# Kernel optimization log

Hardware: AMD Instinct MI355X
Metric: run time of the kernel (lower is better)

Reference implementation:

```python
import jax, jax.numpy as jnp
import numpy as np

# Dims mirror cfg: hidden_dim=128, n_cluster=512; margin from cfg['memory_bank']
B, D, H, W = 64, 128, 64, 64
K = 512
MARGIN = 0.005
EPS = 1e-12  # F.normalize eps


def setup_inputs() -> dict:
    key = jax.random.key(0)
    k1, k2 = jax.random.split(key)
    x = jax.random.normal(k1, (B, D, H, W), dtype=jnp.float32)
    centroid = jax.random.normal(k2, (K, D), dtype=jnp.float32)
    return {"x": x, "centroid": centroid}


def _l2_normalize(v, axis=-1):
    n = jnp.sqrt(jnp.sum(v * v, axis=axis, keepdims=True))
    return v / jnp.maximum(n, EPS)


def reference(x, centroid):
    b, d, h, w = x.shape
    # _flatten: (b,d,h,w) -> (bhw, d)
    flat_raw = jnp.transpose(x, (0, 2, 3, 1)).reshape(-1, d)  # (N, d)
    norm_x = _l2_normalize(flat_raw)                          # (N, d), F.normalize(dim=-1)
    c_norm = _l2_normalize(centroid)                          # (K, d)

    dist = (jnp.sum(norm_x * norm_x, axis=1, keepdims=True)
            + jnp.sum(c_norm * c_norm, axis=1)
            - 2.0 * jnp.matmul(norm_x, c_norm.T))

    idx = jnp.argmin(dist, axis=-1)                           # (N,) hard assignment
    neg_top2, _ = jax.lax.top_k(-dist, 2)                     # torch.topk(-distance, k=2)
    gap = neg_top2[:, 0] - neg_top2[:, 1]                     # values[:,0]-values[:,1]
    above = gap > MARGIN                                      # margin mask

    # masked per-cluster scatter of the RAW features (the enqueue step),
    # expressed as a fixed-shape segment reduction instead of ragged queues.
    sel = jnp.where(above[:, None], flat_raw, 0.0)            # (N, d)
    cluster_sums = jax.ops.segment_sum(sel, idx, num_segments=K)            # (K, d)
    counts = jax.ops.segment_sum(above.astype(jnp.float32), idx, num_segments=K)  # (K,)

    # _reshape(norm_z1_1): (bhw, d) -> (b, d, h, w)
    out = jnp.transpose(norm_x.reshape(b, h, w, d), (0, 3, 1, 2))
    return out, cluster_sums, counts, idx
```

## Files before the change

### kernel.cpp

```cpp
#include <hip/hip_runtime.h>
#include <stdint.h>

#define D 128
#define K 512
#define HW 4096
#define NPIX 262144
#define OUT_NORM_ELEMS 33554432
#define MARGIN 0.005f
#define EPS 1e-12f
#define LOSCALE 2048.0f
#define RSCALE (1.0f / 2048.0f)

typedef _Float16 f16x8 __attribute__((ext_vector_type(8)));
typedef float f32x4 __attribute__((ext_vector_type(4)));
typedef float f32x2 __attribute__((ext_vector_type(2)));

#define FENCE() asm volatile("" ::: "memory")

__device__ __forceinline__ short f2h(float f) {
    _Float16 h = (_Float16)f; return *reinterpret_cast<short*>(&h);
}
__device__ __forceinline__ float h2f(short s) {
    _Float16 h = *reinterpret_cast<_Float16*>(&s); return (float)h;
}

__global__ void zero_kernel(float* __restrict__ p, int n) {
    int i = blockIdx.x * blockDim.x + threadIdx.x;
    if (i < n) p[i] = 0.0f;
}

__global__ void normalize_centroids(const float* __restrict__ c,
                                    short* __restrict__ csp,
                                    float* __restrict__ nc) {
    int k = blockIdx.x * 4 + (threadIdx.x >> 6);
    int lane = threadIdx.x & 63;
    float2 v = *(const float2*)(c + (size_t)k * D + lane * 2);
    float ss = v.x * v.x + v.y * v.y;
    #pragma unroll
    for (int off = 32; off; off >>= 1) ss += __shfl_xor(ss, off);
    float rinv = 1.0f / fmaxf(sqrtf(ss), EPS);
    float ox = v.x * rinv, oy = v.y * rinv;
    short hx = f2h(ox), hy = f2h(oy);
    short lx = f2h((ox - h2f(hx)) * LOSCALE);
    short ly = f2h((oy - h2f(hy)) * LOSCALE);
    *(short2*)&csp[(size_t)k * 256 + 2 * lane]       = make_short2(hx, hy);
    *(short2*)&csp[(size_t)k * 256 + 128 + 2 * lane] = make_short2(lx, ly);
    float ss2 = ox * ox + oy * oy;
    #pragma unroll
    for (int off = 32; off; off >>= 1) ss2 += __shfl_xor(ss2, off);
    if (lane == 0) nc[k] = ss2;
}

#define K1S 66
__global__ __launch_bounds__(256) void normalize_x(
    const float* __restrict__ x, float* __restrict__ out_norm,
    float* __restrict__ rows, int prim)
{
    __shared__ float xt[256 * K1S];
    const int t = threadIdx.x;
    const int pix0 = blockIdx.x * 256;
    const int b = pix0 >> 12;
    const int p0 = pix0 & (HW - 1);
    const float* xg = x + (size_t)b * (D * HW) + p0 + t;
    float* og = out_norm + (size_t)b * (D * HW) + p0 + t;

    float ss = 0.f;
    #pragma unroll 16
    for (int d = 0; d < D; ++d) { float v = xg[(size_t)d * HW]; ss += v * v; }
    float rinv = 1.f / fmaxf(sqrtf(ss), EPS);

    if (prim) {
        #pragma unroll
        for (int half = 0; half < 2; ++half) {
            const int d0 = half * 64;
            #pragma unroll 8
            for (int d = 0; d < 64; ++d) {
                float v = xg[(size_t)(d0 + d) * HW];
                og[(size_t)(d0 + d) * HW] = v * rinv;
                xt[t * K1S + d] = v;
            }
            __syncthreads();
            #pragma unroll
            for (int s = 0; s < 32; ++s) {
                int idx = s * 256 + t;
                int p = idx >> 5;
                int i = idx & 31;
                f32x2 v = *(f32x2*)&xt[p * K1S + 2 * i];
                *(f32x2*)&rows[(size_t)(pix0 + p) * 128 + d0 + 2 * i] = v;
            }
            __syncthreads();
        }
    } else {
        #pragma unroll 16
        for (int d = 0; d < D; ++d) {
            float v = xg[(size_t)d * HW];
            og[(size_t)d * HW] = v * rinv;
        }
    }
}

#define UPD(dd, cc, ri) do {                                      \
    bool lt1 = (dd) < d1[ri];                                     \
    float nd2 = lt1 ? d1[ri] : (((dd) < d2[ri]) ? (dd) : d2[ri]); \
    i1[ri] = lt1 ? (cc) : i1[ri];                                 \
    d1[ri] = lt1 ? (dd) : d1[ri];                                 \
    d2[ri] = nd2;                                                 \
} while (0)

#define SMBUF 8192
#define SMNC  32768
#define SM2_BYTES 34816
__global__ __launch_bounds__(512, 4) void gemm_top2(
    const float* __restrict__ xn, const float* __restrict__ rows,
    const short* __restrict__ csp, const float* __restrict__ nc,
    float* __restrict__ oidx, int* __restrict__ pixinfo, int prim)
{
    __shared__ char smem[SM2_BYTES] __attribute__((aligned(16)));
    float* nc_s = (float*)(smem + SMNC);

    const int t = threadIdx.x;
    const int lane = t & 63;
    const int wid = t >> 6;
    const int lb15 = lane & 15;
    const int kl4 = lane >> 4;
    const int kl = kl4 * 16;
    const int lswzB = lb15 << 4;
    const int pix0 = blockIdx.x * 256;

    nc_s[t] = nc[t];

    auto stageB = [&](int bufoff, int cb) {
        const char* src = (const char*)csp + (size_t)cb * 512;
        int Pl = wid * 1024 + lane * 16;
        int row = Pl >> 9;
        int goff = Pl ^ ((row & 15) << 4);
        __builtin_amdgcn_global_load_lds(
            (const __attribute__((address_space(1))) uint32_t*)(src + goff),
            (__attribute__((address_space(3))) uint32_t*)(smem + bufoff + Pl),
            16, 0, 0);
    };

    f16x8 ahi[2][4], alo[2][4];
    if (prim) {
        #pragma unroll
        for (int mf = 0; mf < 2; ++mf) {
            const float* rp = rows + (size_t)(pix0 + wid * 32 + mf * 16 + lb15) * 128;
            f32x4 v0[4], v1[4];
            float ss = 0.f;
            #pragma unroll
            for (int kq = 0; kq < 4; ++kq) {
                v0[kq] = *(const f32x4*)(rp + kq * 32 + kl4 * 8);
                v1[kq] = *(const f32x4*)(rp + kq * 32 + kl4 * 8 + 4);
                #pragma unroll
                for (int e = 0; e < 4; ++e)
                    ss += v0[kq][e] * v0[kq][e] + v1[kq][e] * v1[kq][e];
            }
            ss += __shfl_xor(ss, 16);
            ss += __shfl_xor(ss, 32);
            float rinv = 1.f / fmaxf(sqrtf(ss), EPS);
            #pragma unroll
            for (int kq = 0; kq < 4; ++kq) {
                f16x8 h, l;
                #pragma unroll
                for (int e = 0; e < 4; ++e) {
                    float a = v0[kq][e] * rinv;
                    _Float16 hv = (_Float16)a;
                    h[e] = hv; l[e] = (_Float16)((a - (float)hv) * LOSCALE);
                    float c = v1[kq][e] * rinv;
                    _Float16 hw = (_Float16)c;
                    h[4 + e] = hw; l[4 + e] = (_Float16)((c - (float)hw) * LOSCALE);
                }
                ahi[mf][kq] = h; alo[mf][kq] = l;
            }
        }
    } else {
        #pragma unroll
        for (int mf = 0; mf < 2; ++mf) {
            int px = pix0 + wid * 32 + mf * 16 + lb15;
            const float* xp = xn + (size_t)(px >> 12) * (D * HW) + (px & (HW - 1));
            #pragma unroll
            for (int kq = 0; kq < 4; ++kq) {
                f16x8 h, l;
                #pragma unroll
                for (int e = 0; e < 8; ++e) {
                    float v = xp[(size_t)(kq * 32 + kl4 * 8 + e) * HW];
                    _Float16 hv = (_Float16)v;
                    h[e] = hv;
                    l[e] = (_Float16)((v - (float)hv) * LOSCALE);
                }
                ahi[mf][kq] = h; alo[mf][kq] = l;
            }
        }
    }
    __syncthreads();

    stageB(0 * SMBUF, 0);
    stageB(1 * SMBUF, 16);

    float d1[8], d2[8]; int i1[8];
    #pragma unroll
    for (int r = 0; r < 8; ++r) { d1[r] = 3.4e38f; d2[r] = 3.4e38f; i1[r] = 0; }

    for (int c = 0; c < 32; ++c) {
        const int cb = c * 16;
        if (c + 2 < 32) stageB(((c + 2) & 3) * SMBUF, cb + 32);
        if (c < 30)      { asm volatile("s_waitcnt vmcnt(2)" ::: "memory"); }
        else if (c == 30){ asm volatile("s_waitcnt vmcnt(1)" ::: "memory"); }
        else             { asm volatile("s_waitcnt vmcnt(0)" ::: "memory"); }
        __builtin_amdgcn_s_barrier();
        FENCE();
        const int bufoff = (c & 3) * SMBUF;

        f32x4 am[2], ac[2];
        #pragma unroll
        for (int mf = 0; mf < 2; ++mf) {
            am[mf] = (f32x4){0.f, 0.f, 0.f, 0.f};
            ac[mf] = (f32x4){0.f, 0.f, 0.f, 0.f};
        }

        #pragma unroll
        for (int kq = 0; kq < 4; ++kq) {
            const int rowb = lb15 * 512;
            f16x8 bh = *(const f16x8*)(smem + bufoff + rowb + ((kq * 64 + kl) ^ lswzB));
            f16x8 bl = *(const f16x8*)(smem + bufoff + rowb + ((256 + kq * 64 + kl) ^ lswzB));
            #pragma unroll
            for (int mf = 0; mf < 2; ++mf) {
                am[mf] = __builtin_amdgcn_mfma_f32_16x16x32_f16(ahi[mf][kq], bh, am[mf], 0, 0, 0);
                ac[mf] = __builtin_amdgcn_mfma_f32_16x16x32_f16(ahi[mf][kq], bl, ac[mf], 0, 0, 0);
                ac[mf] = __builtin_amdgcn_mfma_f32_16x16x32_f16(alo[mf][kq], bh, ac[mf], 0, 0, 0);
            }
        }

        {
            int cid = cb + lb15;
            float ncv = nc_s[cid];
            #pragma unroll
            for (int mf = 0; mf < 2; ++mf)
                #pragma unroll
                for (int j = 0; j < 4; ++j) {
                    int ri = mf * 4 + j;
                    float dd = ncv - 2.f * am[mf][j] - (2.f * RSCALE) * ac[mf][j];
                    UPD(dd, cid, ri);
                }
        }
        FENCE();
    }

    #pragma unroll
    for (int r = 0; r < 8; ++r) {
        #pragma unroll
        for (int m = 1; m < 16; m <<= 1) {
            float o1 = __shfl_xor(d1[r], m);
            float o2 = __shfl_xor(d2[r], m);
            int   oi = __shfl_xor(i1[r], m);
            bool take = (o1 < d1[r]) || (o1 == d1[r] && oi < i1[r]);
            float loser = take ? d1[r] : o1;
            d2[r] = fminf(loser, fminf(d2[r], o2));
            if (take) { d1[r] = o1; i1[r] = oi; }
        }
    }
    if (lb15 == 0) {
        #pragma unroll
        for (int mf = 0; mf < 2; ++mf)
            #pragma unroll
            for (int j = 0; j < 4; ++j) {
                int r = mf * 4 + j;
                int px = pix0 + wid * 32 + mf * 16 + kl4 * 4 + j;
                oidx[px] = (float)i1[r];
                pixinfo[px] = (d2[r] - d1[r] > MARGIN) ? i1[r] : -1;
            }
    }
}

__global__ __launch_bounds__(256) void segsum_kernel(
    const float* __restrict__ x, const float* __restrict__ rows,
    const int* __restrict__ pixinfo, float* __restrict__ csum,
    float* __restrict__ ccnt, int prim)
{
    __shared__ float psum[4 * 128];
    __shared__ int pcnt[4];
    const int kc   = blockIdx.x >> 3;
    const int oct  = blockIdx.x & 7;
    const int lane = threadIdx.x & 63;
    const int w    = threadIdx.x >> 6;
    const int base = oct * 32768 + w * 8192;

    float a0 = 0.f, a1 = 0.f;
    int cnt = 0;
    for (int it = 0; it < 128; ++it) {
        int ibase = base + it * 64;
        int v = pixinfo[ibase + lane];
        unsigned long long m = __ballot(v == kc);
        cnt += (int)__popcll(m);
        while (m) {
            int bpos = __builtin_ctzll(m);
            m &= m - 1;
            int pid = ibase + bpos;
            if (prim) {
                f32x2 r = *(const f32x2*)(rows + (size_t)pid * 128 + 2 * lane);
                a0 += r.x;
                a1 += r.y;
            } else {
                const float* xp = x + ((size_t)(pid >> 12)) * (D * HW) + (pid & (HW - 1));
                a0 += xp[(size_t)(2 * lane) * HW];
                a1 += xp[(size_t)(2 * lane + 1) * HW];
            }
        }
    }
    psum[w * 128 + 2 * lane]     = a0;
    psum[w * 128 + 2 * lane + 1] = a1;
    if (lane == 0) pcnt[w] = cnt;
    __syncthreads();
    if (threadIdx.x < 128) {
        float s = psum[threadIdx.x] + psum[128 + threadIdx.x] +
                  psum[256 + threadIdx.x] + psum[384 + threadIdx.x];
        atomicAdd(&csum[(size_t)kc * D + threadIdx.x], s);
    }
    if (threadIdx.x == 0) {
        float c = (float)(pcnt[0] + pcnt[1] + pcnt[2] + pcnt[3]);
        atomicAdd(&ccnt[kc], c);
    }
}

extern "C" void kernel_launch(void* const* d_in, const int* in_sizes, int n_in,
                              void* d_out, int out_size, void* d_ws, size_t ws_size,
                              hipStream_t stream) {
    const float* x   = (const float*)d_in[0];
    const float* cen = (const float*)d_in[1];

    float* out      = (float*)d_out;
    float* out_norm = out;
    float* csum     = out + OUT_NORM_ELEMS;
    float* ccnt     = csum + (size_t)K * D;
    float* oidx     = ccnt + K;

    char* ws = (char*)d_ws;
    short* csp     = (short*)ws;
    float* nc      = (float*)(ws + 262144);
    int*   pixinfo = (int*)(ws + 264192);
    float* rows    = (float*)(ws + 1312768);
    const size_t need_prim = 1312768ull + (size_t)NPIX * D * 4;
    int prim = (ws_size >= need_prim) ? 1 : 0;

    hipLaunchKernelGGL(zero_kernel, dim3((K * D + K + 255) / 256), dim3(256), 0, stream,
                       csum, K * D + K);
    hipLaunchKernelGGL(normalize_centroids, dim3(K / 4), dim3(256), 0, stream,
                       cen, csp, nc);
    hipLaunchKernelGGL(normalize_x, dim3(NPIX / 256), dim3(256), 0, stream,
                       x, out_norm, rows, prim);
    hipLaunchKernelGGL(gemm_top2, dim3(NPIX / 256), dim3(512), 0, stream,
                       out_norm, rows, csp, nc, oidx, pixinfo, prim);
    hipLaunchKernelGGL(segsum_kernel, dim3(K * 8), dim3(256), 0, stream,
                       x, rows, pixinfo, csum, ccnt, prim);
}
```

Before: 342.0 us.

## Stage full pixel tile in LDS so normalize_x reads input once

normalize_x now loads the whole 256-pixel by 128-channel tile into shared memory with coalesced float2 loads. It then computes per-pixel norms from LDS and writes both the normalized NCHW output and the pixel-major rows copy from that staged tile. The old path streamed x from global memory twice: once for the sum of squares and again for the writes. Block size goes to 512 threads, and the fallback path splits each pixel's reduction across two threads. The tile takes about 130KB of LDS, which allows only one block per CU and may reduce latency hiding.

```diff
diff --git a/kernel.cpp b/kernel.cpp
--- a/kernel.cpp
+++ b/kernel.cpp
@@ -51,50 +51,72 @@
     if (lane == 0) nc[k] = ss2;
 }
 
-#define K1S 66
-__global__ __launch_bounds__(256) void normalize_x(
+#define K1S 129
+__global__ __launch_bounds__(512) void normalize_x(
     const float* __restrict__ x, float* __restrict__ out_norm,
     float* __restrict__ rows, int prim)
 {
     __shared__ float xt[256 * K1S];
+    __shared__ float rinv_s[256];
     const int t = threadIdx.x;
     const int pix0 = blockIdx.x * 256;
     const int b = pix0 >> 12;
     const int p0 = pix0 & (HW - 1);
-    const float* xg = x + (size_t)b * (D * HW) + p0 + t;
-    float* og = out_norm + (size_t)b * (D * HW) + p0 + t;
-
-    float ss = 0.f;
-    #pragma unroll 16
-    for (int d = 0; d < D; ++d) { float v = xg[(size_t)d * HW]; ss += v * v; }
-    float rinv = 1.f / fmaxf(sqrtf(ss), EPS);
+    const float* xg = x + (size_t)b * (D * HW) + p0;
+    float* og = out_norm + (size_t)b * (D * HW) + p0;
 
     if (prim) {
-        #pragma unroll
-        for (int half = 0; half < 2; ++half) {
-            const int d0 = half * 64;
-            #pragma unroll 8
-            for (int d = 0; d < 64; ++d) {
-                float v = xg[(size_t)(d0 + d) * HW];
-                og[(size_t)(d0 + d) * HW] = v * rinv;
-                xt[t * K1S + d] = v;
-            }
-            __syncthreads();
-            #pragma unroll
-            for (int s = 0; s < 32; ++s) {
-                int idx = s * 256 + t;
-                int p = idx >> 5;
-                int i = idx & 31;
-                f32x2 v = *(f32x2*)&xt[p * K1S + 2 * i];
-                *(f32x2*)&rows[(size_t)(pix0 + p) * 128 + d0 + 2 * i] = v;
-            }
-            __syncthreads();
+        #pragma unroll 8
+        for (int s = 0; s < 32; ++s) {
+            int gid = s * 512 + t;
+            int d = gid >> 7;
+            int px2 = (gid & 127) * 2;
+            f32x2 v = *(const f32x2*)(xg + (size_t)d * HW + px2);
+            xt[(px2 + 0) * K1S + d] = v.x;
+            xt[(px2 + 1) * K1S + d] = v.y;
+        }
+        __syncthreads();
+        {
+            int px = t >> 1, half = t & 1;
+            float ss = 0.f;
+            #pragma unroll 16
+            for (int i = 0; i < 64; ++i) {
+                float v = xt[px * K1S + half * 64 + i];
+                ss += v * v;
+            }
+            ss += __shfl_xor(ss, 1);
+            if (half == 0) rinv_s[px] = 1.f / fmaxf(sqrtf(ss), EPS);
+        }
+        __syncthreads();
+        #pragma unroll 8
+        for (int s = 0; s < 64; ++s) {
+            int idx = s * 512 + t;
+            int d = idx >> 8;
+            int px = idx & 255;
+            og[(size_t)d * HW + px] = xt[px * K1S + d] * rinv_s[px];
+        }
+        #pragma unroll 8
+        for (int s = 0; s < 64; ++s) {
+            int idx = s * 512 + t;
+            int px = idx >> 7;
+            int c = idx & 127;
+            rows[(size_t)(pix0 + px) * 128 + c] = xt[px * K1S + c];
         }
     } else {
+        int px = t >> 1, half = t & 1;
+        const float* xp = xg + px;
+        float ss = 0.f;
         #pragma unroll 16
-        for (int d = 0; d < D; ++d) {
-            float v = xg[(size_t)d * HW];
-            og[(size_t)d * HW] = v * rinv;
+        for (int d = 0; d < 64; ++d) {
+            float v = xp[(size_t)(half * 64 + d) * HW];
+            ss += v * v;
+        }
+        ss += __shfl_xor(ss, 1);
+        float rinv = 1.f / fmaxf(sqrtf(ss), EPS);
+        #pragma unroll 16
+        for (int d = 0; d < 64; ++d) {
+            float v = xp[(size_t)(half * 64 + d) * HW];
+            og[(size_t)(half * 64 + d) * HW + px] = v * rinv;
         }
     }
 }
@@ -346,7 +368,7 @@
                        csum, K * D + K);
     hipLaunchKernelGGL(normalize_centroids, dim3(K / 4), dim3(256), 0, stream,
                        cen, csp, nc);
-    hipLaunchKernelGGL(normalize_x, dim3(NPIX / 256), dim3(256), 0, stream,
+    hipLaunchKernelGGL(normalize_x, dim3(NPIX / 256), dim3(512), 0, stream,
                        x, out_norm, rows, prim);
     hipLaunchKernelGGL(gemm_top2, dim3(NPIX / 256), dim3(512), 0, stream,
                        out_norm, rows, csp, nc, oidx, pixinfo, prim);
```

Result: faster. 318.0 us (-7.0%).
